# Kernel optimization log

Measured on AMD Instinct MI355X. Metric: run time of the kernel, lower is better.

The kernel has to match this reference:

```python
import jax, jax.numpy as jnp
import numpy as np
from jax import lax

NUM_TAGS = 126
T = NUM_TAGS + 2          # tag_size = 128
B, S = 256, 512
START, STOP = T - 3, T - 2
NEG = -10000.0


def setup_inputs() -> dict:
    key = jax.random.key(0)
    k1, k2, k3 = jax.random.split(key, 3)
    feats = jax.random.normal(k1, (B, S, T), jnp.float32)
    # learned transition matrix with the module's init masking pattern
    trans = jax.random.normal(k2, (T, T), jnp.float32)
    trans = trans.at[:, START].set(NEG).at[STOP, :].set(NEG)
    trans = trans.at[:, 0].set(NEG).at[0, :].set(NEG)
    # prefix masks with varying valid lengths in [S/2, S]
    lengths = jax.random.randint(k3, (B,), S // 2, S + 1)
    mask = jnp.arange(S)[None, :] < lengths[:, None]
    return {"feats": feats, "mask": mask, "transitions": trans}


def reference(feats, mask, transitions):
    # Viterbi decode (module.forward returns (None, decode_idx)).
    Bn, Sn, Tn = feats.shape
    start, stop = Tn - 3, Tn - 2
    emit = jnp.transpose(feats, (1, 0, 2))            # (S, B, T)
    m = jnp.transpose(mask.astype(jnp.int32))         # (S, B)
    lengths = mask.astype(jnp.int32).sum(axis=1)      # (B,)

    part0 = emit[0] + transitions[start][None, :]     # (B, T)

    def step(part, inp):
        e_t, m_t = inp
        # scores[t, b, i, j] = feats[t, b, j] + transitions[i, j]
        cur = part[:, :, None] + transitions[None, :, :] + e_t[:, None, :]  # (B, from, to)
        new_part = cur.max(axis=1)                                          # (B, T)
        bp = jnp.argmax(cur, axis=1).astype(jnp.int32)                      # (B, T)
        bp = jnp.where(m_t[:, None] > 0, bp, 0)
        return new_part, (new_part, bp)

    _, (hist, bps) = lax.scan(step, part0, (emit[1:], m[1:]))
    part_hist = jnp.concatenate([part0[None], hist], axis=0)                # (S, B, T)
    back_points = jnp.concatenate(
        [bps, jnp.zeros((1, Bn, Tn), jnp.int32)], axis=0)                   # (S, B, T)

    bidx = jnp.arange(Bn)
    last_pos = lengths - 1                                                  # (B,)
    last_partition = part_hist[last_pos, bidx]                              # (B, T)
    last_bp = jnp.argmax(last_partition[:, :, None] + transitions[None], axis=1)
    pointer = last_bp[:, stop].astype(jnp.int32)                            # (B,)

    # overwrite back_points at the last valid position with the final pointer
    bp_bt = jnp.transpose(back_points, (1, 0, 2))                           # (B, S, T)
    bp_bt = bp_bt.at[bidx, last_pos].set(
        jnp.broadcast_to(pointer[:, None], (Bn, Tn)))
    back_points = jnp.transpose(bp_bt, (1, 0, 2))                           # (S, B, T)

    def trace(ptr, bp_t):
        new_ptr = jnp.take_along_axis(bp_t, ptr[:, None], axis=1)[:, 0]
        return new_ptr, new_ptr

    _, rev = lax.scan(trace, pointer, back_points[:-1], reverse=True)       # (S-1, B)
    decode = jnp.concatenate([rev, pointer[None]], axis=0)                  # (S, B)
    return jnp.transpose(decode)                                            # (B, S)
```

## Files before the change

kernel.cpp:

```cpp
#include <hip/hip_runtime.h>
#include <cstdint>
#include <cstddef>

constexpr int T_ = 128;
constexpr int S_ = 512;
constexpr int B_ = 256;
constexpr int START_ = T_ - 3;
constexpr int STOP_  = T_ - 2;
constexpr float NEGINF_ = -3.402823466e38f;

__device__ __forceinline__ void lds_barrier() {
  asm volatile("s_waitcnt lgkmcnt(0)\n\ts_barrier" ::: "memory");
}

__device__ __forceinline__ float readlane_f(float v, int sl) {
  return __int_as_float(__builtin_amdgcn_readlane(__float_as_int(v), sl));
}

__device__ __forceinline__ float ig_reduce_max(float m) {
  int x = __builtin_amdgcn_mov_dpp(__float_as_int(m), 0xB1, 0xF, 0xF, true);
  m = fmaxf(m, __int_as_float(x));
  x = __builtin_amdgcn_mov_dpp(__float_as_int(m), 0x4E, 0xF, 0xF, true);
  m = fmaxf(m, __int_as_float(x));
  x = __builtin_amdgcn_mov_dpp(__float_as_int(m), 0x141, 0xF, 0xF, true);
  m = fmaxf(m, __int_as_float(x));
  return m;
}

__global__ __launch_bounds__(256, 1) void viterbi_forward(
    const float* __restrict__ feats,
    const float* __restrict__ trans,
    float* __restrict__ ph)
{
  const int tid  = threadIdx.x;
  const int lane = tid & 63;
  const int w    = tid >> 6;
  const int ig   = lane & 7;
  const int jl   = lane >> 3;
  const int jg   = w * 8 + jl;
  const int j0   = jg * 4;
  const int b    = blockIdx.x;

  __shared__ alignas(16) float part[2][160];

  float4 tc[16];
  #pragma unroll
  for (int ii = 0; ii < 16; ++ii)
    tc[ii] = *(const float4*)&trans[(16 * ig + ii) * T_ + j0];

  const float* fb = feats + (size_t)b * S_ * T_;
  const int woff = j0 + 4 * (jg >> 2);

  float4 e0 = *(const float4*)&fb[j0];
  float4 ts = *(const float4*)&trans[START_ * T_ + j0];
  float4 p0 = make_float4(e0.x + ts.x, e0.y + ts.y, e0.z + ts.z, e0.w + ts.w);
  if (ig == 0) {
    *(float4*)&part[0][woff] = p0;
    *(float4*)&ph[(size_t)b * T_ + j0] = p0;
  }
  float4 e_next = *(const float4*)&fb[T_ + j0];
  __syncthreads();

  for (int t = 1; t < S_; ++t) {
    float4 e_cur = e_next;
    if (t + 1 < S_) e_next = *(const float4*)&fb[(size_t)(t + 1) * T_ + j0];

    const float4* p4 = (const float4*)part[(t - 1) & 1];
    float4 p[4];
    #pragma unroll
    for (int q = 0; q < 4; ++q) p[q] = p4[5 * ig + q];

    float m0 = NEGINF_, m1 = NEGINF_, m2 = NEGINF_, m3 = NEGINF_;
    #pragma unroll
    for (int q = 0; q < 4; ++q) {
      float4 pv = p[q];
      float4 t0 = tc[4 * q + 0], t1 = tc[4 * q + 1];
      float4 t2 = tc[4 * q + 2], t3 = tc[4 * q + 3];
      m0 = fmaxf(m0, fmaxf(fmaxf(pv.x + t0.x, pv.y + t1.x),
                           fmaxf(pv.z + t2.x, pv.w + t3.x)));
      m1 = fmaxf(m1, fmaxf(fmaxf(pv.x + t0.y, pv.y + t1.y),
                           fmaxf(pv.z + t2.y, pv.w + t3.y)));
      m2 = fmaxf(m2, fmaxf(fmaxf(pv.x + t0.z, pv.y + t1.z),
                           fmaxf(pv.z + t2.z, pv.w + t3.z)));
      m3 = fmaxf(m3, fmaxf(fmaxf(pv.x + t0.w, pv.y + t1.w),
                           fmaxf(pv.z + t2.w, pv.w + t3.w)));
    }
    float4 np4 = make_float4(ig_reduce_max(m0) + e_cur.x,
                             ig_reduce_max(m1) + e_cur.y,
                             ig_reduce_max(m2) + e_cur.z,
                             ig_reduce_max(m3) + e_cur.w);
    if (ig == 0) *(float4*)&part[t & 1][woff] = np4;
    lds_barrier();
    if (ig == 0)
      *(float4*)&ph[((size_t)t * B_ + b) * T_ + j0] = np4;
  }
}

constexpr int CH_ = 8;
constexpr int TS_ = 130;

__global__ __launch_bounds__(64, 1) void viterbi_trace(
    const float* __restrict__ feats,
    const void*  __restrict__ mask,
    const float* __restrict__ trans,
    const float* __restrict__ ph,
    int* __restrict__ out)
{
  const int b    = blockIdx.x;
  const int lane = threadIdx.x;

  __shared__ alignas(16) float transT[T_ * TS_];
  #pragma unroll 4
  for (int g = lane; g < T_ * T_; g += 64) {
    int i = g >> 7, jj = g & (T_ - 1);
    transT[jj * TS_ + i] = trans[g];
  }
  __syncthreads();

  int len = 0;
  {
    const int w0 = *(const int*)mask;
    if (w0 == 0x01010101) {
      const unsigned char* m = (const unsigned char*)mask + (size_t)b * S_;
      for (int s = lane; s < S_; s += 64) len += (m[s] != 0);
    } else if (w0 == 0x3F800000) {
      const float* m = (const float*)mask + (size_t)b * S_;
      for (int s = lane; s < S_; s += 64) len += (m[s] != 0.0f);
    } else {
      const int* m = (const int*)mask + (size_t)b * S_;
      for (int s = lane; s < S_; s += 64) len += (m[s] != 0);
    }
    #pragma unroll
    for (int o = 32; o > 0; o >>= 1) len += __shfl_xor(len, o);
  }
  const int lp = len - 1;

  const float2 L = *(const float2*)(ph + ((size_t)lp * B_ + b) * T_ + 2 * lane);
  float v0 = L.x + transT[STOP_ * TS_ + 2 * lane];
  float v1 = L.y + transT[STOP_ * TS_ + 2 * lane + 1];
  float mx = fmaxf(v0, v1);
  #pragma unroll
  for (int o = 32; o > 0; o >>= 1) mx = fmaxf(mx, __shfl_xor(mx, o));
  {
    unsigned long long g0 = __ballot(v0 == mx);
    unsigned long long g1 = __ballot(v1 == mx);
    int p0 = g0 ? 2 * (__ffsll(g0) - 1)     : (1 << 30);
    int p1 = g1 ? 2 * (__ffsll(g1) - 1) + 1 : (1 << 30);
    int pointer = min(p0, p1);

    for (int k = lp + 1 + lane; k <= S_ - 2; k += 64) out[b * S_ + k] = 0;
    if (lane == 0) {
      out[b * S_ + (S_ - 1)] = pointer;
      if (lp < S_ - 1) out[b * S_ + lp] = pointer;
    }

    int   ptr = pointer;
    float tg  = readlane_f((ptr & 1) ? L.y : L.x, ptr >> 1);
    const float* fb = feats + (size_t)b * S_ * T_;
    const float2 FL = *(const float2*)(fb + (size_t)lp * T_ + 2 * lane);
    float e = readlane_f((ptr & 1) ? FL.y : FL.x, ptr >> 1);

    float2 PA[CH_], FA[CH_], PB[CH_], FB[CH_];

    auto issue = [&](float2 (&P)[CH_], float2 (&F)[CH_], int k0) {
      #pragma unroll
      for (int s = 0; s < CH_; ++s) {
        int k = k0 - s; if (k < 0) k = 0;
        P[s] = *(const float2*)(ph + ((size_t)k * B_ + b) * T_ + 2 * lane);
        F[s] = *(const float2*)(fb + (size_t)k * T_ + 2 * lane);
      }
    };
    auto process = [&](const float2 (&P)[CH_], const float2 (&F)[CH_], int k0) {
      #pragma unroll
      for (int s = 0; s < CH_; ++s) {
        const int k = k0 - s;
        if (k >= 0) {
          const float2 tr = *(const float2*)(transT + ptr * TS_ + 2 * lane);
          float cx = (P[s].x + tr.x) + e;
          float cy = (P[s].y + tr.y) + e;
          unsigned long long q0 = __ballot(cx == tg);
          unsigned long long q1 = __ballot(cy == tg);
          int a0 = q0 ? 2 * (__ffsll(q0) - 1)     : (1 << 30);
          int a1 = q1 ? 2 * (__ffsll(q1) - 1) + 1 : (1 << 30);
          ptr = min(a0, a1);
          if (lane == 0) out[b * S_ + k] = ptr;
          tg = readlane_f((ptr & 1) ? P[s].y : P[s].x, ptr >> 1);
          e  = readlane_f((ptr & 1) ? F[s].y : F[s].x, ptr >> 1);
        }
      }
    };

    issue(PA, FA, lp - 1);
    for (int k0 = lp - 1; k0 >= 0; k0 -= 2 * CH_) {
      issue(PB, FB, k0 - CH_);
      process(PA, FA, k0);
      issue(PA, FA, k0 - 2 * CH_);
      process(PB, FB, k0 - CH_);
    }
  }
}

extern "C" void kernel_launch(void* const* d_in, const int* in_sizes, int n_in,
                              void* d_out, int out_size, void* d_ws, size_t ws_size,
                              hipStream_t stream) {
  const float* feats = (const float*)d_in[0];
  const void*  mask  = d_in[1];
  const float* trans = (const float*)d_in[2];
  float* ph = (float*)d_ws;
  int*   out = (int*)d_out;

  viterbi_forward<<<dim3(B_), dim3(256), 0, stream>>>(feats, trans, ph);
  viterbi_trace  <<<dim3(B_), dim3(64), 0, stream>>>(feats, mask, trans, ph, out);
}
```

Before: 455.3 us.

## Split Viterbi forward step across 512 threads and prefetch emissions in batches

The forward kernel now uses 512 threads per batch element. Each group of 16 lanes reduces over 8 source tags per lane instead of 8 lanes over 16, which halves the per-thread register transition tile and the serial max chain per time step, at the cost of one more DPP reduction stage. Emission loads are now prefetched four steps ahead with double-buffered register arrays instead of one step ahead, to hide global latency on the sequential recurrence. The larger block means each per-step barrier now synchronizes 8 waves instead of 4.

Result: faster. 414.7 us (-8.9%).

```diff
diff --git a/kernel.cpp b/kernel.cpp
--- a/kernel.cpp
+++ b/kernel.cpp
@@ -7,7 +7,6 @@
 constexpr int B_ = 256;
 constexpr int START_ = T_ - 3;
 constexpr int STOP_  = T_ - 2;
-constexpr float NEGINF_ = -3.402823466e38f;
 
 __device__ __forceinline__ void lds_barrier() {
   asm volatile("s_waitcnt lgkmcnt(0)\n\ts_barrier" ::: "memory");
@@ -17,39 +16,39 @@
   return __int_as_float(__builtin_amdgcn_readlane(__float_as_int(v), sl));
 }
 
-__device__ __forceinline__ float ig_reduce_max(float m) {
+__device__ __forceinline__ float ig16_rmax(float m) {
   int x = __builtin_amdgcn_mov_dpp(__float_as_int(m), 0xB1, 0xF, 0xF, true);
   m = fmaxf(m, __int_as_float(x));
   x = __builtin_amdgcn_mov_dpp(__float_as_int(m), 0x4E, 0xF, 0xF, true);
   m = fmaxf(m, __int_as_float(x));
   x = __builtin_amdgcn_mov_dpp(__float_as_int(m), 0x141, 0xF, 0xF, true);
   m = fmaxf(m, __int_as_float(x));
+  x = __builtin_amdgcn_mov_dpp(__float_as_int(m), 0x140, 0xF, 0xF, true);
+  m = fmaxf(m, __int_as_float(x));
   return m;
 }
 
-__global__ __launch_bounds__(256, 1) void viterbi_forward(
+__global__ __launch_bounds__(512, 2) void viterbi_forward(
     const float* __restrict__ feats,
     const float* __restrict__ trans,
     float* __restrict__ ph)
 {
+  const int b    = blockIdx.x;
   const int tid  = threadIdx.x;
   const int lane = tid & 63;
-  const int w    = tid >> 6;
-  const int ig   = lane & 7;
-  const int jl   = lane >> 3;
-  const int jg   = w * 8 + jl;
+  const int ig   = lane & 15;
+  const int jg   = tid >> 4;
   const int j0   = jg * 4;
-  const int b    = blockIdx.x;
-
-  __shared__ alignas(16) float part[2][160];
-
-  float4 tc[16];
+
+  __shared__ alignas(16) float part[2][192];
+
+  float4 tc[8];
   #pragma unroll
-  for (int ii = 0; ii < 16; ++ii)
-    tc[ii] = *(const float4*)&trans[(16 * ig + ii) * T_ + j0];
+  for (int ii = 0; ii < 8; ++ii)
+    tc[ii] = *(const float4*)&trans[(8 * ig + ii) * T_ + j0];
 
   const float* fb = feats + (size_t)b * S_ * T_;
-  const int woff = j0 + 4 * (jg >> 2);
+  const int woff  = j0 + 4 * (j0 >> 3);
 
   float4 e0 = *(const float4*)&fb[j0];
   float4 ts = *(const float4*)&trans[START_ * T_ + j0];
@@ -58,41 +57,55 @@
     *(float4*)&part[0][woff] = p0;
     *(float4*)&ph[(size_t)b * T_ + j0] = p0;
   }
-  float4 e_next = *(const float4*)&fb[T_ + j0];
   __syncthreads();
 
-  for (int t = 1; t < S_; ++t) {
-    float4 e_cur = e_next;
-    if (t + 1 < S_) e_next = *(const float4*)&fb[(size_t)(t + 1) * T_ + j0];
-
+  auto stepf = [&](int t, float4 e4) {
     const float4* p4 = (const float4*)part[(t - 1) & 1];
-    float4 p[4];
-    #pragma unroll
-    for (int q = 0; q < 4; ++q) p[q] = p4[5 * ig + q];
-
-    float m0 = NEGINF_, m1 = NEGINF_, m2 = NEGINF_, m3 = NEGINF_;
-    #pragma unroll
-    for (int q = 0; q < 4; ++q) {
-      float4 pv = p[q];
-      float4 t0 = tc[4 * q + 0], t1 = tc[4 * q + 1];
-      float4 t2 = tc[4 * q + 2], t3 = tc[4 * q + 3];
-      m0 = fmaxf(m0, fmaxf(fmaxf(pv.x + t0.x, pv.y + t1.x),
-                           fmaxf(pv.z + t2.x, pv.w + t3.x)));
-      m1 = fmaxf(m1, fmaxf(fmaxf(pv.x + t0.y, pv.y + t1.y),
-                           fmaxf(pv.z + t2.y, pv.w + t3.y)));
-      m2 = fmaxf(m2, fmaxf(fmaxf(pv.x + t0.z, pv.y + t1.z),
-                           fmaxf(pv.z + t2.z, pv.w + t3.z)));
-      m3 = fmaxf(m3, fmaxf(fmaxf(pv.x + t0.w, pv.y + t1.w),
-                           fmaxf(pv.z + t2.w, pv.w + t3.w)));
-    }
-    float4 np4 = make_float4(ig_reduce_max(m0) + e_cur.x,
-                             ig_reduce_max(m1) + e_cur.y,
-                             ig_reduce_max(m2) + e_cur.z,
-                             ig_reduce_max(m3) + e_cur.w);
+    float4 pa = p4[3 * ig];
+    float4 pb = p4[3 * ig + 1];
+    const float pv[8] = {pa.x, pa.y, pa.z, pa.w, pb.x, pb.y, pb.z, pb.w};
+    float m[4];
+    #pragma unroll
+    for (int c = 0; c < 4; ++c) {
+      float a0 = pv[0] + ((const float*)&tc[0])[c];
+      float a1 = pv[1] + ((const float*)&tc[1])[c];
+      float a2 = pv[2] + ((const float*)&tc[2])[c];
+      float a3 = pv[3] + ((const float*)&tc[3])[c];
+      float a4 = pv[4] + ((const float*)&tc[4])[c];
+      float a5 = pv[5] + ((const float*)&tc[5])[c];
+      float a6 = pv[6] + ((const float*)&tc[6])[c];
+      float a7 = pv[7] + ((const float*)&tc[7])[c];
+      float mm = fmaxf(fmaxf(fmaxf(a0, a1), fmaxf(a2, a3)),
+                       fmaxf(fmaxf(a4, a5), fmaxf(a6, a7)));
+      m[c] = ig16_rmax(mm);
+    }
+    float4 np4 = make_float4(m[0] + e4.x, m[1] + e4.y, m[2] + e4.z, m[3] + e4.w);
     if (ig == 0) *(float4*)&part[t & 1][woff] = np4;
     lds_barrier();
     if (ig == 0)
       *(float4*)&ph[((size_t)t * B_ + b) * T_ + j0] = np4;
+  };
+
+  float4 EA[4], EB[4];
+  #pragma unroll
+  for (int u = 0; u < 4; ++u)
+    EA[u] = *(const float4*)&fb[(size_t)(1 + u) * T_ + j0];
+
+  for (int t0 = 1; t0 < S_; t0 += 8) {
+    #pragma unroll
+    for (int u = 0; u < 4; ++u) {
+      int tr = t0 + 4 + u; if (tr > S_ - 1) tr = S_ - 1;
+      EB[u] = *(const float4*)&fb[(size_t)tr * T_ + j0];
+    }
+    #pragma unroll
+    for (int u = 0; u < 4; ++u) { int t = t0 + u; if (t < S_) stepf(t, EA[u]); }
+    #pragma unroll
+    for (int u = 0; u < 4; ++u) {
+      int tr = t0 + 8 + u; if (tr > S_ - 1) tr = S_ - 1;
+      EA[u] = *(const float4*)&fb[(size_t)tr * T_ + j0];
+    }
+    #pragma unroll
+    for (int u = 0; u < 4; ++u) { int t = t0 + 4 + u; if (t < S_) stepf(t, EB[u]); }
   }
 }
 
@@ -209,6 +222,6 @@
   float* ph = (float*)d_ws;
   int*   out = (int*)d_out;
 
-  viterbi_forward<<<dim3(B_), dim3(256), 0, stream>>>(feats, trans, ph);
+  viterbi_forward<<<dim3(B_), dim3(512), 0, stream>>>(feats, trans, ph);
   viterbi_trace  <<<dim3(B_), dim3(64), 0, stream>>>(feats, mask, trans, ph, out);
 }
```
